# Optimization experiments

Hardware: AMD Instinct MI355X
Metric: run time of the kernel (lower is better)

The kernel has to match this reference:

```python
import jax, jax.numpy as jnp
import numpy as np

N, E, F_IN, EF, HID = 100000, 1600000, 32, 8, 16


def gat_conv(x, W, att_src, att_dst, b, src, dst, heads, out_ch):
    # PyG GATConv: h = x@W per head; score = LeakyReLU(a_s.h_src + a_d.h_dst);
    # segment-softmax over incoming edges of each dst; weighted sum of h_src.
    n = x.shape[0]
    h = (x @ W).reshape(n, heads, out_ch)                      # [N,H,C]
    a_s = jnp.sum(h * att_src, axis=-1)                        # [N,H]
    a_d = jnp.sum(h * att_dst, axis=-1)                        # [N,H]
    e = jax.nn.leaky_relu(a_s[src] + a_d[dst], 0.2)            # [E',H]
    m = jax.ops.segment_max(e, dst, num_segments=n)            # [N,H]
    ex = jnp.exp(e - m[dst])
    denom = jax.ops.segment_sum(ex, dst, num_segments=n)
    alpha = ex / (denom[dst] + 1e-16)                          # [E',H]
    out = jax.ops.segment_sum(h[src] * alpha[:, :, None], dst, num_segments=n)
    return out.reshape(n, heads * out_ch) + b


def setup_inputs() -> dict:
    key = jax.random.key(0)
    ks = jax.random.split(key, 16)
    s = 0.1
    return {
        "x": jax.random.normal(ks[0], (N, F_IN), jnp.float32),
        "edge_index": jax.random.randint(ks[1], (2, E), 0, N, jnp.int32),
        "edge_attr": jax.random.uniform(ks[2], (E, 2 * EF), jnp.float32),
        "num_edge_features": EF,
        "num_edge_masks": EF,
        # conv1: heads=4, out=16
        "W1": jax.random.normal(ks[3], (F_IN, 4 * HID), jnp.float32) * s,
        "att_src1": jax.random.normal(ks[4], (4, HID), jnp.float32) * s,
        "att_dst1": jax.random.normal(ks[5], (4, HID), jnp.float32) * s,
        "b1": jnp.zeros((4 * HID,), jnp.float32),
        # conv2: heads=1, out=16
        "W2": jax.random.normal(ks[6], (4 * HID, HID), jnp.float32) * s,
        "att_src2": jax.random.normal(ks[7], (1, HID), jnp.float32) * s,
        "att_dst2": jax.random.normal(ks[8], (1, HID), jnp.float32) * s,
        "b2": jnp.zeros((HID,), jnp.float32),
        # edge MLP
        "mlp_W1": jax.random.normal(ks[9], (EF, HID), jnp.float32) * s,
        "mlp_b1": jnp.zeros((HID,), jnp.float32),
        "mlp_W2": jax.random.normal(ks[10], (HID, HID), jnp.float32) * s,
        "mlp_b2": jnp.zeros((HID,), jnp.float32),
        # fc_edge: 3*hid -> 1
        "fc_W": jax.random.normal(ks[11], (3 * HID, 1), jnp.float32) * s,
        "fc_b": jnp.zeros((1,), jnp.float32),
    }


def reference(x, edge_index, edge_attr, num_edge_features, num_edge_masks,
              W1, att_src1, att_dst1, b1, W2, att_src2, att_dst2, b2,
              mlp_W1, mlp_b1, mlp_W2, mlp_b2, fc_W, fc_b):
    n = x.shape[0]
    src, dst = edge_index[0], edge_index[1]
    # GATConv adds self loops internally (PyG default)
    loops = jnp.arange(n, dtype=edge_index.dtype)
    src_sl = jnp.concatenate([src, loops])
    dst_sl = jnp.concatenate([dst, loops])
    ef = edge_attr[:, :num_edge_features] * edge_attr[:, num_edge_features:]
    h = gat_conv(x, W1, att_src1, att_dst1, b1, src_sl, dst_sl, 4, HID)
    h = jax.nn.elu(h)                                          # dropout: eval mode -> identity
    h = gat_conv(h, W2, att_src2, att_dst2, b2, src_sl, dst_sl, 1, HID)
    ef = jax.nn.relu(ef @ mlp_W1 + mlp_b1) @ mlp_W2 + mlp_b2   # edge MLP
    emb = jnp.concatenate([h[src], h[dst], ef], axis=1)        # [E,3*HID]
    return (emb @ fc_W + fc_b).squeeze(-1)                     # [E]
```

## Files before the change

### kernel.cpp

```cpp
#include <hip/hip_runtime.h>
#include <hip/hip_bf16.h>
#include <hip/hip_fp16.h>


#define FIN 32
#define C1 64
#define HID 16
#define BSH 8
#define CAP2 6144
#define SOP 68

__device__ __forceinline__ float leaky02(float x) {
    return x > 0.f ? x : 0.2f * x;
}

__global__ void k_binit3(int* __restrict__ bcur, int nbuck) {
    int b = blockIdx.x * blockDim.x + threadIdx.x;
    if (b < nbuck) bcur[b] = b * CAP2;
}

__global__ void __launch_bounds__(256) k_binF(
        const int* __restrict__ src, const int* __restrict__ dst,
        int* __restrict__ bcur, unsigned* __restrict__ brec,
        const float* __restrict__ ea,
        const float* __restrict__ mlpW1, const float* __restrict__ mlpb1,
        const float* __restrict__ mlpW2, const float* __restrict__ mlpb2,
        const float* __restrict__ fcW, const float* __restrict__ fcb,
        float* __restrict__ outp,
        int e, int ep, int nbuck, int gbin) {
    __shared__ int cnt[512];
    __shared__ int cur[512];
    __shared__ float sW[128];
    __shared__ float sb[16];
    __shared__ float sw2[17];
    int tid = threadIdx.x;
    if ((int)blockIdx.x < gbin) {
        int cb = blockIdx.x * 4096;
        for (int j = tid; j < 512; j += 256) cnt[j] = 0;
        __syncthreads();
        unsigned rec[16];
        int bk[16];
#pragma unroll
        for (int t = 0; t < 16; t++) {
            int i = cb + t * 256 + tid;
            bk[t] = -1;
            if (i < ep) {
                int s, d;
                if (i < e) { s = src[i]; d = dst[i]; }
                else       { s = i - e; d = s; }
                int b = d >> BSH;
                rec[t] = ((unsigned)(d & 255) << 17) | (unsigned)s;
                bk[t] = b;
                atomicAdd(&cnt[b], 1);
            }
        }
        __syncthreads();
        for (int b = tid; b < nbuck; b += 256) {
            int c = cnt[b];
            cur[b] = (c > 0) ? atomicAdd(&bcur[b], c) : 0;
        }
        __syncthreads();
#pragma unroll
        for (int t = 0; t < 16; t++) {
            if (bk[t] >= 0) {
                int p = atomicAdd(&cur[bk[t]], 1);
                if (p < (bk[t] + 1) * CAP2)
                    brec[p] = rec[t];
            }
        }
    } else {
        if (tid < 128) sW[tid] = mlpW1[tid];
        if (tid < 16)  sb[tid] = mlpb1[tid];
        if (tid < 16) {
            float s = 0.f;
#pragma unroll
            for (int k = 0; k < 16; k++) s += mlpW2[tid * 16 + k] * fcW[32 + k];
            sw2[tid] = s;
        } else if (tid == 16) {
            float s = fcb[0];
            for (int k = 0; k < 16; k++) s += mlpb2[k] * fcW[32 + k];
            sw2[16] = s;
        }
        __syncthreads();
        int eid = ((int)blockIdx.x - gbin) * 256 + tid;
        if (eid >= e) return;
        const float4* ev = (const float4*)ea + (size_t)eid * 4;
        float4 v0 = ev[0], v1 = ev[1], v2 = ev[2], v3 = ev[3];
        float ef[8] = { v0.x * v2.x, v0.y * v2.y, v0.z * v2.z, v0.w * v2.w,
                        v1.x * v3.x, v1.y * v3.y, v1.z * v3.z, v1.w * v3.w };
        float acc = sw2[16];
#pragma unroll
        for (int j = 0; j < 16; j++) {
            float tt = sb[j];
#pragma unroll
            for (int i = 0; i < 8; i++) tt += ef[i] * sW[i * 16 + j];
            acc += fmaxf(tt, 0.f) * sw2[j];
        }
        outp[eid] = acc;
    }
}

__global__ void __launch_bounds__(256) k_fineF(
        const unsigned* __restrict__ brec, const int* __restrict__ bcur,
        int* __restrict__ offs, int* __restrict__ oend, int* __restrict__ ssrc,
        const float* __restrict__ x, const float* __restrict__ W1,
        const float* __restrict__ att_s, const float* __restrict__ att_d,
        __half* __restrict__ h1h, float* __restrict__ a1, float* __restrict__ d1,
        int n, int gfine) {
    __shared__ int lcnt[256];
    __shared__ int sbuf[256];
    __shared__ float sW[FIN * C1];
    __shared__ float sA[C1], sD[C1];
    __shared__ float sX[4 * FIN];
    int tid = threadIdx.x;
    if ((int)blockIdx.x < gfine) {
        int b = blockIdx.x;
        int n0 = b << BSH;
        int base = b * CAP2;
        int cnt = min(bcur[b] - base, CAP2);
        lcnt[tid] = 0;
        __syncthreads();
        for (int i = tid; i < cnt; i += 256) {
            unsigned r = brec[base + i];
            atomicAdd(&lcnt[r >> 17], 1);
        }
        __syncthreads();
        int v = lcnt[tid];
        sbuf[tid] = v;
        __syncthreads();
        for (int off = 1; off < 256; off <<= 1) {
            int u = (tid >= off) ? sbuf[tid - off] : 0;
            __syncthreads();
            sbuf[tid] += u;
            __syncthreads();
        }
        int excl = sbuf[tid] - v;
        if (n0 + tid < n) {
            offs[n0 + tid] = base + excl;
            oend[n0 + tid] = base + excl + v;
        }
        lcnt[tid] = base + excl;
        __syncthreads();
        for (int i = tid; i < cnt; i += 256) {
            unsigned r = brec[base + i];
            int p = atomicAdd(&lcnt[r >> 17], 1);
            ssrc[p] = (int)(r & 0x1FFFF);
        }
    } else {
        int nb = (int)blockIdx.x - gfine;
        for (int i = tid; i < FIN * C1; i += 256) sW[i] = W1[i];
        if (tid < C1) { sA[tid] = att_s[tid]; sD[tid] = att_d[tid]; }
        int bse = nb * 4;
        if (tid < 4 * FIN) {
            int nn = bse + (tid >> 5);
            sX[tid] = (nn < n) ? x[(size_t)nn * FIN + (tid & 31)] : 0.f;
        }
        __syncthreads();
        int li = tid >> 6, c = tid & 63;
        int node = bse + li;
        if (node >= n) return;
        const float* xr = sX + li * FIN;
        float acc = 0.f;
#pragma unroll
        for (int k = 0; k < FIN; k++) acc += xr[k] * sW[k * C1 + c];
        h1h[(size_t)node * C1 + c] = __float2half(acc);
        float pa = acc * sA[c], pb = acc * sD[c];
#pragma unroll
        for (int m = 8; m >= 1; m >>= 1) {
            pa += __shfl_xor(pa, m, 16);
            pb += __shfl_xor(pb, m, 16);
        }
        if ((c & 15) == 0) {
            a1[node * 4 + (c >> 4)] = pa;
            d1[node * 4 + (c >> 4)] = pb;
        }
    }
}

__global__ void __launch_bounds__(256) k_agg1F(
        const __half* __restrict__ h1h, const float* __restrict__ a1,
        const float* __restrict__ d1, const float* __restrict__ b1,
        const float* __restrict__ W2,
        const float* __restrict__ att_s2, const float* __restrict__ att_d2,
        const int* __restrict__ offs, const int* __restrict__ oend,
        const int* __restrict__ ssrc,
        __half* __restrict__ h2h, float* __restrict__ a2, float* __restrict__ d2,
        int n) {
    __shared__ float4 w4l[4][64];
    __shared__ int    sil[4][64];
    __shared__ float  sO[4][2][SOP];
    __shared__ float  sW2[C1 * HID];
    int tid = threadIdx.x;
    for (int i = tid; i < C1 * HID; i += 256) sW2[i] = W2[i];
    __syncthreads();
    int wid = (int)((blockIdx.x * (size_t)blockDim.x + tid) >> 6);
    int lane = tid & 63;
    int wl = tid >> 6;
    int which = lane >> 5;
    int lane32 = lane & 31;
    int node = wid * 2 + which;
    if (node >= n) return;
    int sub = lane32 & 7;
    int g   = lane32 >> 3;
    int head = sub >> 1;
    unsigned lane_off = (unsigned)sub * 16u;
    const char* hb = (const char*)h1h;
    float4 dv = ((const float4*)d1)[node];
    int s0 = offs[node], s1v = oend[node];
    float acc[8] = {0.f, 0.f, 0.f, 0.f, 0.f, 0.f, 0.f, 0.f};
    float dsum = 0.f;
    for (int base = s0; base < s1v; base += 32) {
        int cnt = min(32, s1v - base);
        int sl = (lane32 < cnt) ? ssrc[base + lane32] : 0;
        float4 a4 = ((const float4*)a1)[(unsigned)sl];
        float4 w4;
        if (lane32 < cnt) {
            w4.x = __expf(leaky02(a4.x + dv.x));
            w4.y = __expf(leaky02(a4.y + dv.y));
            w4.z = __expf(leaky02(a4.z + dv.z));
            w4.w = __expf(leaky02(a4.w + dv.w));
        } else {
            w4.x = w4.y = w4.z = w4.w = 0.f;
        }
        w4l[wl][lane] = w4;
        sil[wl][lane] = sl << 7;
        __builtin_amdgcn_wave_barrier();
        int cnt4 = (cnt + 3) & ~3;
        int lbase = which << 5;
#pragma unroll 4
        for (int j = g; j < cnt4; j += 4) {
            int soff = sil[wl][lbase + j];
            float w = ((const float*)&w4l[wl][lbase + j])[head];
            float4 raw = *(const float4*)(hb + (unsigned)soff + lane_off);
            float2 f0 = __half22float2(*(__half2*)&raw.x);
            float2 f1 = __half22float2(*(__half2*)&raw.y);
            float2 f2 = __half22float2(*(__half2*)&raw.z);
            float2 f3 = __half22float2(*(__half2*)&raw.w);
            acc[0] = fmaf(w, f0.x, acc[0]);
            acc[1] = fmaf(w, f0.y, acc[1]);
            acc[2] = fmaf(w, f1.x, acc[2]);
            acc[3] = fmaf(w, f1.y, acc[3]);
            acc[4] = fmaf(w, f2.x, acc[4]);
            acc[5] = fmaf(w, f2.y, acc[5]);
            acc[6] = fmaf(w, f3.x, acc[6]);
            acc[7] = fmaf(w, f3.y, acc[7]);
            dsum += w;
        }
        __builtin_amdgcn_wave_barrier();
    }
#pragma unroll
    for (int m = 8; m <= 16; m <<= 1) {
#pragma unroll
        for (int i = 0; i < 8; i++) acc[i] += __shfl_xor(acc[i], m, 64);
        dsum += __shfl_xor(dsum, m, 64);
    }
    if (lane32 < 8) {
        float inv = 1.f / (dsum + 1e-16f);
        float4 bA = ((const float4*)b1)[lane32 * 2];
        float4 bB = ((const float4*)b1)[lane32 * 2 + 1];
        float4 oA, oB;
        oA.x = acc[0] * inv + bA.x;
        oA.y = acc[1] * inv + bA.y;
        oA.z = acc[2] * inv + bA.z;
        oA.w = acc[3] * inv + bA.w;
        oB.x = acc[4] * inv + bB.x;
        oB.y = acc[5] * inv + bB.y;
        oB.z = acc[6] * inv + bB.z;
        oB.w = acc[7] * inv + bB.w;
        oA.x = oA.x > 0.f ? oA.x : (__expf(oA.x) - 1.f);
        oA.y = oA.y > 0.f ? oA.y : (__expf(oA.y) - 1.f);
        oA.z = oA.z > 0.f ? oA.z : (__expf(oA.z) - 1.f);
        oA.w = oA.w > 0.f ? oA.w : (__expf(oA.w) - 1.f);
        oB.x = oB.x > 0.f ? oB.x : (__expf(oB.x) - 1.f);
        oB.y = oB.y > 0.f ? oB.y : (__expf(oB.y) - 1.f);
        oB.z = oB.z > 0.f ? oB.z : (__expf(oB.z) - 1.f);
        oB.w = oB.w > 0.f ? oB.w : (__expf(oB.w) - 1.f);
        *((float4*)&sO[wl][which][lane32 * 8])     = oA;
        *((float4*)&sO[wl][which][lane32 * 8 + 4]) = oB;
    }
    __builtin_amdgcn_wave_barrier();
    int c = lane32 & 15, kh = lane32 >> 4;
    const float* orow = sO[wl][which];
    float part = 0.f;
#pragma unroll
    for (int k = 0; k < 32; k++)
        part += orow[kh * 32 + k] * sW2[(kh * 32 + k) * HID + c];
    part += __shfl_xor(part, 16, 64);
    if (lane32 < 16) h2h[(size_t)node * HID + c] = __float2half(part);
    float pa = part * att_s2[c], pb = part * att_d2[c];
#pragma unroll
    for (int m = 8; m >= 1; m >>= 1) {
        pa += __shfl_xor(pa, m, 64);
        pb += __shfl_xor(pb, m, 64);
    }
    if (lane32 == 0) { a2[node] = pa; d2[node] = pb; }
}

__global__ void __launch_bounds__(256) k_agg2(
        const __half* __restrict__ h2h, const float* __restrict__ a2,
        const float* __restrict__ d2, const float* __restrict__ b2,
        const float* __restrict__ fcW,
        const int* __restrict__ offs, const int* __restrict__ oend,
        const int* __restrict__ ssrc,
        float* __restrict__ ps, float* __restrict__ pd, int n) {
    __shared__ float2 wsl[4][64];
    int wid = (int)((blockIdx.x * (size_t)blockDim.x + threadIdx.x) >> 6);
    int lane = threadIdx.x & 63;
    int wl = threadIdx.x >> 6;
    int which = lane >> 5;
    int lane32 = lane & 31;
    int node = wid * 2 + which;
    if (node >= n) return;
    int sub = lane32 & 1;
    int g   = lane32 >> 1;
    unsigned lane_off = (unsigned)sub * 16u;
    const char* hb = (const char*)h2h;
    float dvv = d2[node];
    int s0 = offs[node], s1v = oend[node];
    float acc[8] = {0.f, 0.f, 0.f, 0.f, 0.f, 0.f, 0.f, 0.f};
    float dsum = 0.f;
    for (int base = s0; base < s1v; base += 32) {
        int cnt = min(32, s1v - base);
        int sl = (lane32 < cnt) ? ssrc[base + lane32] : 0;
        float av = a2[(unsigned)sl];
        float w = (lane32 < cnt) ? __expf(leaky02(av + dvv)) : 0.f;
        wsl[wl][lane] = make_float2(w, __int_as_float(sl << 5));
        __builtin_amdgcn_wave_barrier();
        int cnt16 = (cnt + 15) & ~15;
        int lbase = which << 5;
#pragma unroll 2
        for (int j = g; j < cnt16; j += 16) {
            float2 e0 = wsl[wl][lbase + j];
            unsigned soff = (unsigned)__float_as_int(e0.y);
            float4 raw = *(const float4*)(hb + soff + lane_off);
            float2 f0 = __half22float2(*(__half2*)&raw.x);
            float2 f1 = __half22float2(*(__half2*)&raw.y);
            float2 f2 = __half22float2(*(__half2*)&raw.z);
            float2 f3 = __half22float2(*(__half2*)&raw.w);
            acc[0] = fmaf(e0.x, f0.x, acc[0]);
            acc[1] = fmaf(e0.x, f0.y, acc[1]);
            acc[2] = fmaf(e0.x, f1.x, acc[2]);
            acc[3] = fmaf(e0.x, f1.y, acc[3]);
            acc[4] = fmaf(e0.x, f2.x, acc[4]);
            acc[5] = fmaf(e0.x, f2.y, acc[5]);
            acc[6] = fmaf(e0.x, f3.x, acc[6]);
            acc[7] = fmaf(e0.x, f3.y, acc[7]);
            dsum += e0.x;
        }
        __builtin_amdgcn_wave_barrier();
    }
#pragma unroll
    for (int m = 2; m <= 16; m <<= 1) {
#pragma unroll
        for (int i = 0; i < 8; i++) acc[i] += __shfl_xor(acc[i], m, 64);
        dsum += __shfl_xor(dsum, m, 64);
    }
    float p1 = 0.f, p2 = 0.f;
    if (lane32 < 2) {
        float inv = 1.f / (dsum + 1e-16f);
        float4 bA = ((const float4*)b2)[lane32 * 2];
        float4 bB = ((const float4*)b2)[lane32 * 2 + 1];
        float4 fsA = ((const float4*)fcW)[lane32 * 2];
        float4 fsB = ((const float4*)fcW)[lane32 * 2 + 1];
        float4 fdA = ((const float4*)fcW)[4 + lane32 * 2];
        float4 fdB = ((const float4*)fcW)[4 + lane32 * 2 + 1];
        float h0 = acc[0] * inv + bA.x, h1v = acc[1] * inv + bA.y;
        float h2v = acc[2] * inv + bA.z, h3 = acc[3] * inv + bA.w;
        float h4 = acc[4] * inv + bB.x, h5 = acc[5] * inv + bB.y;
        float h6 = acc[6] * inv + bB.z, h7 = acc[7] * inv + bB.w;
        p1 = h0 * fsA.x + h1v * fsA.y + h2v * fsA.z + h3 * fsA.w
           + h4 * fsB.x + h5 * fsB.y + h6 * fsB.z + h7 * fsB.w;
        p2 = h0 * fdA.x + h1v * fdA.y + h2v * fdA.z + h3 * fdA.w
           + h4 * fdB.x + h5 * fdB.y + h6 * fdB.z + h7 * fdB.w;
    }
    p1 += __shfl_xor(p1, 1, 64);
    p2 += __shfl_xor(p2, 1, 64);
    if (lane32 == 0) { ps[node] = p1; pd[node] = p2; }
}

__global__ void __launch_bounds__(256) k_final2(
        const int* __restrict__ src, const int* __restrict__ dst,
        const float* __restrict__ ps, const float* __restrict__ pd,
        float* __restrict__ out, int e) {
    int eid = blockIdx.x * blockDim.x + threadIdx.x;
    if (eid < e) out[eid] += ps[src[eid]] + pd[dst[eid]];
}

extern "C" void kernel_launch(void* const* d_in, const int* in_sizes, int n_in,
                              void* d_out, int out_size, void* d_ws, size_t ws_size,
                              hipStream_t stream) {
    const float* x        = (const float*)d_in[0];
    const int*   eidx     = (const int*)d_in[1];
    const float* eattr    = (const float*)d_in[2];
    const float* W1       = (const float*)d_in[5];
    const float* att_s1   = (const float*)d_in[6];
    const float* att_d1   = (const float*)d_in[7];
    const float* b1       = (const float*)d_in[8];
    const float* W2       = (const float*)d_in[9];
    const float* att_s2   = (const float*)d_in[10];
    const float* att_d2   = (const float*)d_in[11];
    const float* b2       = (const float*)d_in[12];
    const float* mlp_W1   = (const float*)d_in[13];
    const float* mlp_b1   = (const float*)d_in[14];
    const float* mlp_W2   = (const float*)d_in[15];
    const float* mlp_b2   = (const float*)d_in[16];
    const float* fc_W     = (const float*)d_in[17];
    const float* fc_b     = (const float*)d_in[18];

    const int n = in_sizes[0] / FIN;
    const int e = in_sizes[2] / 16;
    const int ep = e + n;
    const int* src = eidx;
    const int* dst = eidx + e;
    const int nbuck = (n + 255) >> BSH;

    char* p = (char*)d_ws;
    auto carve = [&](size_t bytes) {
        char* r = p;
        p += (bytes + 255) & ~(size_t)255;
        return r;
    };
    __half* h1h  = (__half*)carve((size_t)n * C1 * 2);
    __half* h2h  = (__half*)carve((size_t)n * HID * 2);
    float*  a1   = (float*)carve((size_t)n * 4 * 4);
    float*  d1   = (float*)carve((size_t)n * 4 * 4);
    float*  a2   = (float*)carve((size_t)n * 4);
    float*  d2   = (float*)carve((size_t)n * 4);
    float*  ps   = (float*)carve((size_t)n * 4);
    float*  pd   = (float*)carve((size_t)n * 4);
    int*    offs = (int*)carve((size_t)n * 4);
    int*    oendp= (int*)carve((size_t)n * 4);
    int*    bcur = (int*)carve(512 * 4);
    int*    ssrc = (int*)carve((size_t)nbuck * CAP2 * 4);
    unsigned* brec = (unsigned*)carve((size_t)nbuck * CAP2 * 4);

    float* outp = (float*)d_out;

    const int gbin  = (ep + 4095) / 4096;
    const int gmlp  = (e + 255) / 256;
    const int gnode1 = (n + 3) / 4;
    const int npair = (n + 1) / 2;

    k_binit3<<<2, 256, 0, stream>>>(bcur, nbuck);
    k_binF<<<gbin + gmlp, 256, 0, stream>>>(src, dst, bcur, brec, eattr,
                                            mlp_W1, mlp_b1, mlp_W2, mlp_b2,
                                            fc_W, fc_b, outp, e, ep, nbuck, gbin);
    k_fineF<<<nbuck + gnode1, 256, 0, stream>>>(brec, bcur, offs, oendp, ssrc,
                                                x, W1, att_s1, att_d1,
                                                h1h, a1, d1, n, nbuck);
    k_agg1F<<<(npair * 64 + 255) / 256, 256, 0, stream>>>(
        h1h, a1, d1, b1, W2, att_s2, att_d2, offs, oendp, ssrc, h2h, a2, d2, n);
    k_agg2<<<(npair * 64 + 255) / 256, 256, 0, stream>>>(
        h2h, a2, d2, b2, fc_W, offs, oendp, ssrc, ps, pd, n);
    k_final2<<<(e + 255) / 256, 256, 0, stream>>>(src, dst, ps, pd, outp, e);
}
```

Baseline: 187.1 us.

## Move edge-MLP blocks from binning kernel into layer-1 aggregation kernel

The edge-MLP work, which streams edge_attr and writes the partial per-edge output, was co-scheduled with the edge binning kernel. It now runs as extra trailing blocks of the first GAT aggregation kernel, which is gather-latency bound. The likely intent is to overlap bandwidth-heavy MLP work with a latency-bound kernel and leave binning its own launch. The inner aggregation loop unroll also goes from 4 to 8, which may raise register pressure. The new shared arrays also add LDS per block.

```diff
diff --git a/kernel.cpp b/kernel.cpp
--- a/kernel.cpp
+++ b/kernel.cpp
@@ -19,84 +19,45 @@
     if (b < nbuck) bcur[b] = b * CAP2;
 }
 
-__global__ void __launch_bounds__(256) k_binF(
+__global__ void __launch_bounds__(256) k_bin(
         const int* __restrict__ src, const int* __restrict__ dst,
         int* __restrict__ bcur, unsigned* __restrict__ brec,
-        const float* __restrict__ ea,
-        const float* __restrict__ mlpW1, const float* __restrict__ mlpb1,
-        const float* __restrict__ mlpW2, const float* __restrict__ mlpb2,
-        const float* __restrict__ fcW, const float* __restrict__ fcb,
-        float* __restrict__ outp,
-        int e, int ep, int nbuck, int gbin) {
+        int e, int ep, int nbuck) {
     __shared__ int cnt[512];
     __shared__ int cur[512];
-    __shared__ float sW[128];
-    __shared__ float sb[16];
-    __shared__ float sw2[17];
     int tid = threadIdx.x;
-    if ((int)blockIdx.x < gbin) {
-        int cb = blockIdx.x * 4096;
-        for (int j = tid; j < 512; j += 256) cnt[j] = 0;
-        __syncthreads();
-        unsigned rec[16];
-        int bk[16];
-#pragma unroll
-        for (int t = 0; t < 16; t++) {
-            int i = cb + t * 256 + tid;
-            bk[t] = -1;
-            if (i < ep) {
-                int s, d;
-                if (i < e) { s = src[i]; d = dst[i]; }
-                else       { s = i - e; d = s; }
-                int b = d >> BSH;
-                rec[t] = ((unsigned)(d & 255) << 17) | (unsigned)s;
-                bk[t] = b;
-                atomicAdd(&cnt[b], 1);
-            }
-        }
-        __syncthreads();
-        for (int b = tid; b < nbuck; b += 256) {
-            int c = cnt[b];
-            cur[b] = (c > 0) ? atomicAdd(&bcur[b], c) : 0;
-        }
-        __syncthreads();
-#pragma unroll
-        for (int t = 0; t < 16; t++) {
-            if (bk[t] >= 0) {
-                int p = atomicAdd(&cur[bk[t]], 1);
-                if (p < (bk[t] + 1) * CAP2)
-                    brec[p] = rec[t];
-            }
-        }
-    } else {
-        if (tid < 128) sW[tid] = mlpW1[tid];
-        if (tid < 16)  sb[tid] = mlpb1[tid];
-        if (tid < 16) {
-            float s = 0.f;
-#pragma unroll
-            for (int k = 0; k < 16; k++) s += mlpW2[tid * 16 + k] * fcW[32 + k];
-            sw2[tid] = s;
-        } else if (tid == 16) {
-            float s = fcb[0];
-            for (int k = 0; k < 16; k++) s += mlpb2[k] * fcW[32 + k];
-            sw2[16] = s;
-        }
-        __syncthreads();
-        int eid = ((int)blockIdx.x - gbin) * 256 + tid;
-        if (eid >= e) return;
-        const float4* ev = (const float4*)ea + (size_t)eid * 4;
-        float4 v0 = ev[0], v1 = ev[1], v2 = ev[2], v3 = ev[3];
-        float ef[8] = { v0.x * v2.x, v0.y * v2.y, v0.z * v2.z, v0.w * v2.w,
-                        v1.x * v3.x, v1.y * v3.y, v1.z * v3.z, v1.w * v3.w };
-        float acc = sw2[16];
-#pragma unroll
-        for (int j = 0; j < 16; j++) {
-            float tt = sb[j];
-#pragma unroll
-            for (int i = 0; i < 8; i++) tt += ef[i] * sW[i * 16 + j];
-            acc += fmaxf(tt, 0.f) * sw2[j];
-        }
-        outp[eid] = acc;
+    int cb = blockIdx.x * 4096;
+    for (int j = tid; j < 512; j += 256) cnt[j] = 0;
+    __syncthreads();
+    unsigned rec[16];
+    int bk[16];
+#pragma unroll
+    for (int t = 0; t < 16; t++) {
+        int i = cb + t * 256 + tid;
+        bk[t] = -1;
+        if (i < ep) {
+            int s, d;
+            if (i < e) { s = src[i]; d = dst[i]; }
+            else       { s = i - e; d = s; }
+            int b = d >> BSH;
+            rec[t] = ((unsigned)(d & 255) << 17) | (unsigned)s;
+            bk[t] = b;
+            atomicAdd(&cnt[b], 1);
+        }
+    }
+    __syncthreads();
+    for (int b = tid; b < nbuck; b += 256) {
+        int c = cnt[b];
+        cur[b] = (c > 0) ? atomicAdd(&bcur[b], c) : 0;
+    }
+    __syncthreads();
+#pragma unroll
+    for (int t = 0; t < 16; t++) {
+        if (bk[t] >= 0) {
+            int p = atomicAdd(&cur[bk[t]], 1);
+            if (p < (bk[t] + 1) * CAP2)
+                brec[p] = rec[t];
+        }
     }
 }
 
@@ -185,12 +146,51 @@
         const int* __restrict__ offs, const int* __restrict__ oend,
         const int* __restrict__ ssrc,
         __half* __restrict__ h2h, float* __restrict__ a2, float* __restrict__ d2,
-        int n) {
+        const float* __restrict__ ea,
+        const float* __restrict__ mlpW1, const float* __restrict__ mlpb1,
+        const float* __restrict__ mlpW2, const float* __restrict__ mlpb2,
+        const float* __restrict__ fcW, const float* __restrict__ fcb,
+        float* __restrict__ outp,
+        int n, int e, int gagg) {
     __shared__ float4 w4l[4][64];
     __shared__ int    sil[4][64];
     __shared__ float  sO[4][2][SOP];
     __shared__ float  sW2[C1 * HID];
+    __shared__ float  sWm[128];
+    __shared__ float  sbm[16];
+    __shared__ float  sw2m[17];
     int tid = threadIdx.x;
+    if ((int)blockIdx.x >= gagg) {
+        if (tid < 128) sWm[tid] = mlpW1[tid];
+        if (tid < 16)  sbm[tid] = mlpb1[tid];
+        if (tid < 16) {
+            float s = 0.f;
+#pragma unroll
+            for (int k = 0; k < 16; k++) s += mlpW2[tid * 16 + k] * fcW[32 + k];
+            sw2m[tid] = s;
+        } else if (tid == 16) {
+            float s = fcb[0];
+            for (int k = 0; k < 16; k++) s += mlpb2[k] * fcW[32 + k];
+            sw2m[16] = s;
+        }
+        __syncthreads();
+        int eid = ((int)blockIdx.x - gagg) * 256 + tid;
+        if (eid >= e) return;
+        const float4* ev = (const float4*)ea + (size_t)eid * 4;
+        float4 v0 = ev[0], v1 = ev[1], v2 = ev[2], v3 = ev[3];
+        float ef[8] = { v0.x * v2.x, v0.y * v2.y, v0.z * v2.z, v0.w * v2.w,
+                        v1.x * v3.x, v1.y * v3.y, v1.z * v3.z, v1.w * v3.w };
+        float acc = sw2m[16];
+#pragma unroll
+        for (int j = 0; j < 16; j++) {
+            float tt = sbm[j];
+#pragma unroll
+            for (int i = 0; i < 8; i++) tt += ef[i] * sWm[i * 16 + j];
+            acc += fmaxf(tt, 0.f) * sw2m[j];
+        }
+        outp[eid] = acc;
+        return;
+    }
     for (int i = tid; i < C1 * HID; i += 256) sW2[i] = W2[i];
     __syncthreads();
     int wid = (int)((blockIdx.x * (size_t)blockDim.x + tid) >> 6);
@@ -227,7 +227,7 @@
         __builtin_amdgcn_wave_barrier();
         int cnt4 = (cnt + 3) & ~3;
         int lbase = which << 5;
-#pragma unroll 4
+#pragma unroll 8
         for (int j = g; j < cnt4; j += 4) {
             int soff = sil[wl][lbase + j];
             float w = ((const float*)&w4l[wl][lbase + j])[head];
@@ -440,16 +440,16 @@
     const int gmlp  = (e + 255) / 256;
     const int gnode1 = (n + 3) / 4;
     const int npair = (n + 1) / 2;
+    const int gagg  = (npair * 64 + 255) / 256;
 
     k_binit3<<<2, 256, 0, stream>>>(bcur, nbuck);
-    k_binF<<<gbin + gmlp, 256, 0, stream>>>(src, dst, bcur, brec, eattr,
-                                            mlp_W1, mlp_b1, mlp_W2, mlp_b2,
-                                            fc_W, fc_b, outp, e, ep, nbuck, gbin);
+    k_bin<<<gbin, 256, 0, stream>>>(src, dst, bcur, brec, e, ep, nbuck);
     k_fineF<<<nbuck + gnode1, 256, 0, stream>>>(brec, bcur, offs, oendp, ssrc,
                                                 x, W1, att_s1, att_d1,
                                                 h1h, a1, d1, n, nbuck);
-    k_agg1F<<<(npair * 64 + 255) / 256, 256, 0, stream>>>(
-        h1h, a1, d1, b1, W2, att_s2, att_d2, offs, oendp, ssrc, h2h, a2, d2, n);
+    k_agg1F<<<gagg + gmlp, 256, 0, stream>>>(
+        h1h, a1, d1, b1, W2, att_s2, att_d2, offs, oendp, ssrc, h2h, a2, d2,
+        eattr, mlp_W1, mlp_b1, mlp_W2, mlp_b2, fc_W, fc_b, outp, n, e, gagg);
     k_agg2<<<(npair * 64 + 255) / 256, 256, 0, stream>>>(
         h2h, a2, d2, b2, fc_W, offs, oendp, ssrc, ps, pd, n);
     k_final2<<<(e + 255) / 256, 256, 0, stream>>>(src, dst, ps, pd, outp, e);
```

New measurement: 239.6 us. 28.0% more time.
